# Optimization experiments

Measured on AMD Instinct MI355X. Metric: run time of the kernel, lower is better.

## Reference

```python
import jax, jax.numpy as jnp
import numpy as np

B, N, D = 64, 784, 768
H, HD, G = 32, 24, 2
HID = 3072
SCALE = HD ** -0.5
EPS = 1e-6


def _ln(x, g, b):
    m = jnp.mean(x, -1, keepdims=True)
    v = jnp.mean((x - m) ** 2, -1, keepdims=True)
    return (x - m) * jax.lax.rsqrt(v + EPS) * g + b


def setup_inputs() -> dict:
    key = jax.random.key(0)
    ks = jax.random.split(key, 12)
    def rn(k, shape, s=0.02):
        return (jax.random.normal(k, shape) * s).astype(jnp.float32)
    return {
        'x_cls': jax.random.normal(ks[0], (B, 1, D), jnp.float32),
        'x_img': jax.random.normal(ks[1], (B, N, D), jnp.float32),
        'ln1_g': jnp.ones((D,), jnp.float32), 'ln1_b': jnp.zeros((D,), jnp.float32),
        'Wq': rn(ks[2], (D, D)), 'bq': jnp.zeros((D,), jnp.float32),
        'Wk': rn(ks[3], (D, D)), 'bk': jnp.zeros((D,), jnp.float32),
        'Wv': rn(ks[4], (D, D)), 'bv': jnp.zeros((D,), jnp.float32),
        'w1_W': rn(ks[5], (H, H), 0.1), 'w1_b': jnp.zeros((H,), jnp.float32),
        'w2_W': rn(ks[6], (H, H), 0.1), 'w2_b': jnp.zeros((H,), jnp.float32),
        'proj_W': rn(ks[7], (D, D)), 'proj_b': jnp.zeros((D,), jnp.float32),
        'ln2_g': jnp.ones((D,), jnp.float32), 'ln2_b': jnp.zeros((D,), jnp.float32),
        'fc1_W': rn(ks[8], (G, HID // G, D // G)), 'fc1_b': jnp.zeros((G, HID // G), jnp.float32),
        'fc2_W': rn(ks[9], (G, D // G, HID // G)), 'fc2_b': jnp.zeros((G, D // G), jnp.float32),
    }


def reference(x_cls, x_img, ln1_g, ln1_b, Wq, bq, Wk, bk, Wv, bv,
              w1_W, w1_b, w2_W, w2_b, proj_W, proj_b, ln2_g, ln2_b,
              fc1_W, fc1_b, fc2_W, fc2_b):
    # --- ClassAttention (non-mismatch path), dropout = identity (eval) ---
    u = jnp.concatenate([x_cls, x_img], axis=1)  # [B, M, D], M = N+1
    M = u.shape[1]
    n = _ln(u, ln1_g, ln1_b)
    q = ((n[:, :1] @ Wq + bq).reshape(B, 1, H, HD).transpose(0, 2, 1, 3)) * SCALE  # [B,H,1,HD]
    k = (n @ Wk + bk).reshape(B, M, H, HD).transpose(0, 2, 1, 3)                   # [B,H,M,HD]
    v = (n @ Wv + bv).reshape(B, M, H, HD).transpose(0, 2, 1, 3)
    attn = jnp.einsum('bhqd,bhkd->bhqk', q, k)  # [B,H,1,M]
    # interactive score mixing across heads (w1 pre-softmax, w2 post-softmax)
    attn = attn + jnp.einsum('bhqk,hg->bgqk', attn, w1_W) + w1_b[None, :, None, None]
    attn = jax.nn.softmax(attn, axis=-1)
    attn = attn + jnp.einsum('bhqk,hg->bgqk', attn, w2_W) + w2_b[None, :, None, None]
    o = jnp.einsum('bhqk,bhkd->bhqd', attn, v).transpose(0, 2, 1, 3).reshape(B, 1, D)
    x_cls = x_cls + (o @ proj_W + proj_b)
    # --- GroupConvMlp on the cls token (grouped 1x1 convs + channel shuffle) ---
    y = _ln(x_cls, ln2_g, ln2_b)
    h = jnp.einsum('btgc,goc->btgo', y.reshape(B, 1, G, D // G), fc1_W) + fc1_b  # group-major out channels
    h = jax.nn.gelu(h.reshape(B, 1, HID), approximate=False)
    # channel_shuffle(group=G): out channel b*gc+a = in channel a*G+b
    h = h.reshape(B, 1, HID // G, G).transpose(0, 1, 3, 2).reshape(B, 1, HID)
    z = jnp.einsum('btgc,goc->btgo', h.reshape(B, 1, G, HID // G), fc2_W) + fc2_b
    x_cls = x_cls + z.reshape(B, 1, D)
    return (x_cls, x_img)
```

## Files before the change

### kernel.cpp

```cpp
#include <hip/hip_runtime.h>
#include <hip/hip_bf16.h>
#include <math.h>

#define BB   64
#define NN   784
#define DD   768
#define HH   32
#define HD24 24
#define MM   785
#define HIDN 3072
#define QSCALE 0.20412414523193154f
#define LNEPS 1e-6f

#define WS_Q     0
#define WS_RS    49152
#define WS_RM    100352
#define WS_S1P   151552
#define WS_BQP   163840
#define WS_LMX   176128
#define WS_LSM   184320
#define WS_A2P   192512
#define WS_WMP   200704
#define WS_PS    208896
#define WS_C1    210432
#define WS_H2    259584
#define WS_O     456192
#define WS_E     505344
#define WS_T     2143744
#define WS_T2    3751424
#define WS_SLQ   5359104
#define WS_KSEND 5563904
#define WS_ZP    0

typedef __attribute__((ext_vector_type(8))) short bf16x8;
typedef __attribute__((ext_vector_type(4))) float f32x4;

__device__ __forceinline__ unsigned packbf(float a, float b) {
  union { __hip_bfloat162 h2; unsigned u; } cv;
  cv.h2 = __float22bfloat162_rn(make_float2(a, b));
  return cv.u;
}

__global__ __launch_bounds__(256) void k_q(
    const float* __restrict__ x_cls,
    const float* __restrict__ g1, const float* __restrict__ b1,
    const float* __restrict__ Wq, const float* __restrict__ bq,
    float* __restrict__ ws)
{
  const int b = blockIdx.y;
  const int oc0 = blockIdx.x * 64;
  const int t = threadIdx.x;
  const int lane = t & 63, wid = t >> 6;

  __shared__ __align__(16) float nc_l[DD];
  __shared__ float red4[4][64];
  __shared__ float rS[4], rQ[4];
  __shared__ float musd[2];

  float xv[3];
  float s = 0.f, q2 = 0.f;
#pragma unroll
  for (int k = 0; k < 3; ++k) {
    float v = x_cls[(size_t)b * DD + t + 256 * k];
    xv[k] = v; s += v; q2 += v * v;
  }
#pragma unroll
  for (int off = 1; off < 64; off <<= 1) { s += __shfl_xor(s, off); q2 += __shfl_xor(q2, off); }
  if (lane == 0) { rS[wid] = s; rQ[wid] = q2; }
  __syncthreads();
  if (t == 0) {
    float ss = rS[0] + rS[1] + rS[2] + rS[3];
    float qq = rQ[0] + rQ[1] + rQ[2] + rQ[3];
    float mu = ss * (1.f / DD);
    musd[0] = mu; musd[1] = rsqrtf(qq * (1.f / DD) - mu * mu + LNEPS);
  }
  __syncthreads();
  {
    float mu = musd[0], rs = musd[1];
#pragma unroll
    for (int k = 0; k < 3; ++k) {
      int d = t + 256 * k;
      nc_l[d] = (xv[k] - mu) * rs * g1[d] + b1[d];
    }
  }
  __syncthreads();

  const int oc = t & 63, ks = t >> 6;
  const float* wp = Wq + (size_t)(ks * 192) * DD + oc0 + oc;
  const float* ncp = nc_l + ks * 192;
  float a0 = 0.f, a1 = 0.f, a2 = 0.f, a3 = 0.f;
#pragma unroll 4
  for (int d = 0; d < 192; d += 4) {
    a0 += ncp[d + 0] * wp[(size_t)(d + 0) * DD];
    a1 += ncp[d + 1] * wp[(size_t)(d + 1) * DD];
    a2 += ncp[d + 2] * wp[(size_t)(d + 2) * DD];
    a3 += ncp[d + 3] * wp[(size_t)(d + 3) * DD];
  }
  red4[ks][oc] = (a0 + a1) + (a2 + a3);
  __syncthreads();
  if (t < 64) {
    int ocg = oc0 + t;
    ws[WS_Q + (size_t)b * DD + ocg] =
        (red4[0][t] + red4[1][t] + red4[2][t] + red4[3][t] + bq[ocg]) * QSCALE;
  }
}

__global__ __launch_bounds__(256) void k_gqk(
    const float* __restrict__ g1, const float* __restrict__ b1,
    const float* __restrict__ Wk, const float* __restrict__ w1W,
    float* __restrict__ ws)
{
  const int b = blockIdx.y;
  const int d0 = blockIdx.x * 128;
  const int t = threadIdx.x;

  __shared__ __align__(16) float q_l[DD];
  __shared__ float T1[HH * HH];
  __shared__ float qk_l[128][33];
  __shared__ float pS[8][HH], pB[8][HH];

  for (int i = t; i < DD; i += 256) q_l[i] = ws[WS_Q + (size_t)b * DD + i];
  for (int i = t; i < HH * HH; i += 256) {
    int g = i >> 5, h = i & 31;
    T1[i] = w1W[i] + ((g == h) ? 1.f : 0.f);
  }
  __syncthreads();

  {
    const int dl = t >> 1, gh = t & 1;
    const float4* wr = (const float4*)(Wk + (size_t)(d0 + dl) * DD + gh * 384);
    const float4* qr = (const float4*)(q_l + gh * 384);
#pragma unroll 4
    for (int gg = 0; gg < 16; ++gg) {
      float a = 0.f;
#pragma unroll
      for (int c = 0; c < 6; ++c) {
        float4 w = wr[gg * 6 + c];
        float4 p = qr[gg * 6 + c];
        a += w.x * p.x + w.y * p.y + w.z * p.z + w.w * p.w;
      }
      qk_l[dl][gh * 16 + gg] = a;
    }
  }
  __syncthreads();
  {
    const int h = t & 31, dg = t >> 5;
    float fb[16];
    float s1a = 0.f, bqa = 0.f;
#pragma unroll 2
    for (int dd = 0; dd < 16; ++dd) {
      int dl = dg * 16 + dd;
      float f = 0.f;
#pragma unroll 8
      for (int g = 0; g < HH; ++g) f += qk_l[dl][g] * T1[g * HH + h];
      float gq = g1[d0 + dl] * f;
      fb[dd] = gq;
      s1a += gq;
      bqa += b1[d0 + dl] * qk_l[dl][h];
    }
    const int kstep = (d0 >> 5) + (dg >> 1);
    const int nt = h >> 4;
    const int lane0 = (h & 15) + 32 * (dg & 1);
    uint4* GQB = (uint4*)(ws + WS_E) + (size_t)b * (24 * 2 * 64);
    GQB[(kstep * 2 + nt) * 64 + lane0] =
        make_uint4(packbf(fb[0], fb[1]), packbf(fb[2], fb[3]),
                   packbf(fb[4], fb[5]), packbf(fb[6], fb[7]));
    GQB[(kstep * 2 + nt) * 64 + lane0 + 16] =
        make_uint4(packbf(fb[8], fb[9]), packbf(fb[10], fb[11]),
                   packbf(fb[12], fb[13]), packbf(fb[14], fb[15]));
    pS[dg][h] = s1a; pB[dg][h] = bqa;
  }
  __syncthreads();
  if (t < HH) {
    float s = 0.f, bq = 0.f;
#pragma unroll
    for (int k = 0; k < 8; ++k) { s += pS[k][t]; bq += pB[k][t]; }
    ws[WS_S1P + ((size_t)b * 6 + blockIdx.x) * HH + t] = s;
    ws[WS_BQP + ((size_t)b * 6 + blockIdx.x) * HH + t] = bq;
  }
}

__global__ __launch_bounds__(256) void k_main1(
    const float* __restrict__ x_cls, const float* __restrict__ x_img,
    float* __restrict__ ws)
{
  const int b = blockIdx.y;
  const int m0 = blockIdx.x * 64;
  const int nz = gridDim.z;
  const int kh = blockIdx.z;
  const int t = threadIdx.x;
  const int w = t >> 6;
  const int l = t & 63;
  const int lg = l >> 4;
  const int lm = l & 15;

  const uint4* GQ = (const uint4*)(ws + WS_E) + (size_t)b * (24 * 2 * 64);

  const int arow = m0 + w * 16 + lm;
  const bool av = (arow < MM);
  const int arc = av ? arow : 0;
  const float* asrc = (arc == 0) ? (x_cls + (size_t)b * DD)
                                 : (x_img + ((size_t)b * NN + (arc - 1)) * DD);
  const int nk = 24 / nz;
  const int k0 = kh * nk;

  f32x4 acc0 = {0.f, 0.f, 0.f, 0.f};
  f32x4 acc1 = {0.f, 0.f, 0.f, 0.f};
  float sl = 0.f, sq = 0.f;

#pragma unroll 4
  for (int kst = k0; kst < k0 + nk; ++kst) {
    float4 a0 = make_float4(0.f, 0.f, 0.f, 0.f);
    float4 a1 = make_float4(0.f, 0.f, 0.f, 0.f);
    if (av) {
      a0 = *(const float4*)(asrc + kst * 32 + 8 * lg);
      a1 = *(const float4*)(asrc + kst * 32 + 8 * lg + 4);
    }
    sl += (a0.x + a0.y) + (a0.z + a0.w) + (a1.x + a1.y) + (a1.z + a1.w);
    sq += a0.x*a0.x + a0.y*a0.y + a0.z*a0.z + a0.w*a0.w
        + a1.x*a1.x + a1.y*a1.y + a1.z*a1.z + a1.w*a1.w;
    union { uint4 u; bf16x8 h; } ua, ub0, ub1;
    ua.u = make_uint4(packbf(a0.x, a0.y), packbf(a0.z, a0.w),
                      packbf(a1.x, a1.y), packbf(a1.z, a1.w));
    ub0.u = GQ[(kst * 2 + 0) * 64 + l];
    ub1.u = GQ[(kst * 2 + 1) * 64 + l];
    acc0 = __builtin_amdgcn_mfma_f32_16x16x32_bf16(ua.h, ub0.h, acc0, 0, 0, 0);
    acc1 = __builtin_amdgcn_mfma_f32_16x16x32_bf16(ua.h, ub1.h, acc1, 0, 0, 0);
  }

  sl += __shfl_xor(sl, 16); sl += __shfl_xor(sl, 32);
  sq += __shfl_xor(sq, 16); sq += __shfl_xor(sq, 32);
  if (lg == 0 && av) {
    if (nz == 1) {
      float mu = sl * (1.f / DD);
      float rs = rsqrtf(sq * (1.f / DD) - mu * mu + LNEPS);
      ws[WS_RS + (size_t)b * 800 + arow] = rs;
      ws[WS_RM + (size_t)b * 800 + arow] = rs * mu;
    } else {
      float* slq = ws + WS_SLQ + (((size_t)b * 2 + kh) * 800 + arow) * 2;
      slq[0] = sl; slq[1] = sq;
    }
  }

  float* tb = ws + (kh ? WS_T2 : WS_T) + (size_t)b * MM * HH;
#pragma unroll
  for (int r = 0; r < 4; ++r) {
    int row = m0 + w * 16 + 4 * lg + r;
    if (row < MM) {
      tb[(size_t)row * HH + lm] = acc0[r];
      tb[(size_t)row * HH + 16 + lm] = acc1[r];
    }
  }
}

__global__ __launch_bounds__(256) void k_sm_a(
    const float* __restrict__ bk,
    const float* __restrict__ w1W, const float* __restrict__ w1b,
    float* __restrict__ ws, int ksplit)
{
  const int cx = blockIdx.x, b = blockIdx.y;
  const int t = threadIdx.x;
  const int lane = t & 63, wid = t >> 6;

  __shared__ float T1[HH * HH];
  __shared__ float s1_sh[HH], c0_sh[HH], bq_sh[HH];
  __shared__ float red[4][HH];
  __shared__ float lmax_sh[HH];

  for (int i = t; i < HH * HH; i += 256) {
    int g = i >> 5, h = i & 31;
    T1[i] = w1W[i] + ((g == h) ? 1.f : 0.f);
  }
  if (t < HH) {
    float s1v = 0.f, bqv = 0.f;
#pragma unroll
    for (int p = 0; p < 6; ++p) {
      s1v += ws[WS_S1P + ((size_t)b * 6 + p) * HH + t];
      bqv += ws[WS_BQP + ((size_t)b * 6 + p) * HH + t];
    }
    const float* qp = ws + WS_Q + (size_t)b * DD + t * HD24;
#pragma unroll
    for (int j = 0; j < HD24; ++j) bqv += bk[t * HD24 + j] * qp[j];
    s1_sh[t] = s1v; bq_sh[t] = bqv;
  }
  __syncthreads();
  if (t < HH) {
    float c0 = w1b[t];
#pragma unroll
    for (int g = 0; g < HH; ++g) c0 += T1[g * HH + t] * bq_sh[g];
    c0_sh[t] = c0;
  }
  __syncthreads();

  const int m = cx * 256 + t;
  const bool vm = (m < MM);
  float a1[HH];
  if (vm) {
    const float* tb = ws + WS_T + ((size_t)b * MM + m) * HH;
    const float* tb2 = ws + WS_T2 + ((size_t)b * MM + m) * HH;
    float rs, rm;
    if (ksplit) {
      const float* slq = ws + WS_SLQ + ((size_t)b * 2 * 800 + m) * 2;
      float sl = slq[0] + slq[(size_t)800 * 2];
      float sq = slq[1] + slq[(size_t)800 * 2 + 1];
      float mu = sl * (1.f / DD);
      rs = rsqrtf(sq * (1.f / DD) - mu * mu + LNEPS);
      rm = rs * mu;
      ws[WS_RS + (size_t)b * 800 + m] = rs;
      ws[WS_RM + (size_t)b * 800 + m] = rm;
    } else {
      rs = ws[WS_RS + (size_t)b * 800 + m];
      rm = ws[WS_RM + (size_t)b * 800 + m];
    }
#pragma unroll
    for (int q = 0; q < 8; ++q) {
      float4 tv = *(const float4*)(tb + q * 4);
      if (ksplit) {
        float4 t2 = *(const float4*)(tb2 + q * 4);
        tv.x += t2.x; tv.y += t2.y; tv.z += t2.z; tv.w += t2.w;
      }
      a1[4*q+0] = rs * tv.x - rm * s1_sh[4*q+0] + c0_sh[4*q+0];
      a1[4*q+1] = rs * tv.y - rm * s1_sh[4*q+1] + c0_sh[4*q+1];
      a1[4*q+2] = rs * tv.z - rm * s1_sh[4*q+2] + c0_sh[4*q+2];
      a1[4*q+3] = rs * tv.w - rm * s1_sh[4*q+3] + c0_sh[4*q+3];
    }
  } else {
#pragma unroll
    for (int h = 0; h < HH; ++h) a1[h] = -3.0e38f;
  }
#pragma unroll
  for (int h = 0; h < HH; ++h) {
    float v = a1[h];
#pragma unroll
    for (int off = 1; off < 64; off <<= 1) v = fmaxf(v, __shfl_xor(v, off));
    if (lane == 0) red[wid][h] = v;
  }
  __syncthreads();
  if (t < HH) {
    float v = fmaxf(fmaxf(red[0][t], red[1][t]), fmaxf(red[2][t], red[3][t]));
    lmax_sh[t] = v;
    ws[WS_LMX + ((size_t)b * 4 + cx) * HH + t] = v;
  }
  __syncthreads();
  float* E = ws + WS_E + (size_t)b * (HH * 800);
  if (vm) {
#pragma unroll
    for (int h = 0; h < HH; ++h) {
      float e = __expf(a1[h] - lmax_sh[h]);
      a1[h] = e;
      E[(size_t)h * 800 + m] = e;
    }
  } else {
#pragma unroll
    for (int h = 0; h < HH; ++h) a1[h] = 0.f;
  }
#pragma unroll
  for (int h = 0; h < HH; ++h) {
    float v = a1[h];
#pragma unroll
    for (int off = 1; off < 64; off <<= 1) v += __shfl_xor(v, off);
    if (lane == 0) red[wid][h] = v;
  }
  __syncthreads();
  if (t < HH)
    ws[WS_LSM + ((size_t)b * 4 + cx) * HH + t] = red[0][t] + red[1][t] + red[2][t] + red[3][t];
}

__global__ __launch_bounds__(256) void k_sm_b(
    const float* __restrict__ w2W, const float* __restrict__ w2b,
    float* __restrict__ ws)
{
  const int cx = blockIdx.x, b = blockIdx.y;
  const int t = threadIdx.x;
  const int lane = t & 63, wid = t >> 6;

  __shared__ __align__(16) float T2s[HH * HH];
  __shared__ float inv_sh[HH], w2b_sh[HH];
  __shared__ float red[4][HH];

  if (t < HH) {
    float l0 = ws[WS_LMX + ((size_t)b * 4 + 0) * HH + t];
    float l1 = ws[WS_LMX + ((size_t)b * 4 + 1) * HH + t];
    float l2 = ws[WS_LMX + ((size_t)b * 4 + 2) * HH + t];
    float l3 = ws[WS_LMX + ((size_t)b * 4 + 3) * HH + t];
    float gmax = fmaxf(fmaxf(l0, l1), fmaxf(l2, l3));
    float s = ws[WS_LSM + ((size_t)b * 4 + 0) * HH + t] * __expf(l0 - gmax)
            + ws[WS_LSM + ((size_t)b * 4 + 1) * HH + t] * __expf(l1 - gmax)
            + ws[WS_LSM + ((size_t)b * 4 + 2) * HH + t] * __expf(l2 - gmax)
            + ws[WS_LSM + ((size_t)b * 4 + 3) * HH + t] * __expf(l3 - gmax);
    float lcx = (cx == 0) ? l0 : (cx == 1) ? l1 : (cx == 2) ? l2 : l3;
    inv_sh[t] = __expf(lcx - gmax) / s;
    w2b_sh[t] = w2b[t];
  }
  __syncthreads();
  for (int i = t; i < HH * HH; i += 256) {
    int g = i >> 5, h = i & 31;
    T2s[i] = (w2W[i] + ((g == h) ? 1.f : 0.f)) * inv_sh[g];
  }
  __syncthreads();

  const int m = cx * 256 + t;
  float* E = ws + WS_E + (size_t)b * (HH * 800);
  float4 av[8];
#pragma unroll
  for (int q = 0; q < 8; ++q) av[q] = make_float4(0.f,0.f,0.f,0.f);
  float rm = 0.f;
  if (m < MM) {
    float rs = ws[WS_RS + (size_t)b * 800 + m];
    rm = ws[WS_RM + (size_t)b * 800 + m];
#pragma unroll 4
    for (int g = 0; g < HH; ++g) {
      float eg = E[(size_t)g * 800 + m];
#pragma unroll
      for (int q = 0; q < 8; ++q) {
        float4 t2 = *(const float4*)&T2s[g * HH + q * 4];
        av[q].x += eg * t2.x; av[q].y += eg * t2.y;
        av[q].z += eg * t2.z; av[q].w += eg * t2.w;
      }
    }
#pragma unroll
    for (int q = 0; q < 8; ++q) {
      av[q].x += w2b_sh[q*4+0]; av[q].y += w2b_sh[q*4+1];
      av[q].z += w2b_sh[q*4+2]; av[q].w += w2b_sh[q*4+3];
      E[(size_t)(q*4+0) * 800 + m] = av[q].x * rs;
      E[(size_t)(q*4+1) * 800 + m] = av[q].y * rs;
      E[(size_t)(q*4+2) * 800 + m] = av[q].z * rs;
      E[(size_t)(q*4+3) * 800 + m] = av[q].w * rs;
    }
  } else if (m < 800) {
#pragma unroll
    for (int h = 0; h < HH; ++h) E[(size_t)h * 800 + m] = 0.f;
  }
#pragma unroll
  for (int h = 0; h < HH; ++h) {
    float v = ((const float*)&av[h >> 2])[h & 3];
#pragma unroll
    for (int off = 1; off < 64; off <<= 1) v += __shfl_xor(v, off);
    if (lane == 0) red[wid][h] = v;
  }
  __syncthreads();
  if (t < HH)
    ws[WS_A2P + ((size_t)b * 4 + cx) * HH + t] = red[0][t] + red[1][t] + red[2][t] + red[3][t];
  __syncthreads();
#pragma unroll
  for (int h = 0; h < HH; ++h) {
    float v = ((const float*)&av[h >> 2])[h & 3] * rm;
#pragma unroll
    for (int off = 1; off < 64; off <<= 1) v += __shfl_xor(v, off);
    if (lane == 0) red[wid][h] = v;
  }
  __syncthreads();
  if (t < HH)
    ws[WS_WMP + ((size_t)b * 4 + cx) * HH + t] = red[0][t] + red[1][t] + red[2][t] + red[3][t];
}

__global__ __launch_bounds__(512) void k_wsum(
    const float* __restrict__ x_cls, const float* __restrict__ x_img,
    float* __restrict__ out, float* __restrict__ ws)
{
  const int b = blockIdx.y;
  const int d0 = blockIdx.x * 64;
  const int t = threadIdx.x;
  const int wv = t >> 6;
  const int mh = wv >> 2;
  const int hw = wv & 3;
  const int hb = hw * 8;
  const int dseg = t & 15;
  const int msub = (t >> 4) & 3;
  const int mcBeg = mh * 13;
  const int mcN = 13 - mh;

  __shared__ __align__(16) float w_l[HH][800];
  __shared__ __align__(16) float r_s[HH][68];

  const float* W = ws + WS_E + (size_t)b * (HH * 800);
  float* out_img = out + (size_t)BB * DD;

  {
    const float4* Wf = (const float4*)W;
    float4* wl4 = (float4*)&w_l[0][0];
    for (int i = t; i < (HH * 800) / 4; i += 512) wl4[i] = Wf[i];
  }
  __syncthreads();

  float acc[8][4];
#pragma unroll
  for (int j = 0; j < 8; ++j)
#pragma unroll
    for (int c = 0; c < 4; ++c) acc[j][c] = 0.f;

  float4 pu[8], pun[8];

  auto LOADU = [&](int j, float4* dst) {
#pragma unroll
    for (int i = 0; i < 8; ++i) {
      int m = (mcBeg + j) * 32 + msub * 8 + i;
      if (m < MM) {
        const float* src = (m == 0) ? (x_cls + (size_t)b * DD)
                                    : (x_img + ((size_t)b * NN + (m - 1)) * DD);
        dst[i] = *(const float4*)(src + d0 + dseg * 4);
      } else dst[i] = make_float4(0.f,0.f,0.f,0.f);
    }
  };

  LOADU(0, pu);
  for (int j = 0; j < mcN; ++j) {
    if (j + 1 < mcN) LOADU(j + 1, pun);
    const int mbase = (mcBeg + j) * 32 + msub * 8;
#pragma unroll
    for (int jj = 0; jj < 8; ++jj) {
      float4 wA = *(const float4*)&w_l[hb + jj][mbase];
      float4 wB = *(const float4*)&w_l[hb + jj][mbase + 4];
      float wv0 = wA.x, wv1 = wA.y, wv2 = wA.z, wv3 = wA.w;
      float wv4 = wB.x, wv5 = wB.y, wv6 = wB.z, wv7 = wB.w;
      acc[jj][0] += wv0*pu[0].x + wv1*pu[1].x + wv2*pu[2].x + wv3*pu[3].x
                  + wv4*pu[4].x + wv5*pu[5].x + wv6*pu[6].x + wv7*pu[7].x;
      acc[jj][1] += wv0*pu[0].y + wv1*pu[1].y + wv2*pu[2].y + wv3*pu[3].y
                  + wv4*pu[4].y + wv5*pu[5].y + wv6*pu[6].y + wv7*pu[7].y;
      acc[jj][2] += wv0*pu[0].z + wv1*pu[1].z + wv2*pu[2].z + wv3*pu[3].z
                  + wv4*pu[4].z + wv5*pu[5].z + wv6*pu[6].z + wv7*pu[7].z;
      acc[jj][3] += wv0*pu[0].w + wv1*pu[1].w + wv2*pu[2].w + wv3*pu[3].w
                  + wv4*pu[4].w + wv5*pu[5].w + wv6*pu[6].w + wv7*pu[7].w;
    }
#pragma unroll
    for (int i = 0; i < 8; ++i) {
      if ((i >> 1) == hw) {
        int m = (mcBeg + j) * 32 + msub * 8 + i;
        if (m >= 1 && m < MM)
          *(float4*)(out_img + ((size_t)b * NN + (m - 1)) * DD + d0 + dseg * 4) = pu[i];
      }
    }
    if (j + 1 < mcN) {
#pragma unroll
      for (int i = 0; i < 8; ++i) pu[i] = pun[i];
    }
  }

#pragma unroll
  for (int j = 0; j < 8; ++j)
#pragma unroll
    for (int c = 0; c < 4; ++c) {
      float v = acc[j][c];
      v += __shfl_xor(v, 16);
      v += __shfl_xor(v, 32);
      acc[j][c] = v;
    }
  __syncthreads();
  if (mh == 1 && msub == 0) {
#pragma unroll
    for (int j = 0; j < 8; ++j)
      *(float4*)&r_s[hb + j][dseg * 4] =
          make_float4(acc[j][0], acc[j][1], acc[j][2], acc[j][3]);
  }
  __syncthreads();
  if (mh == 0 && msub == 0) {
    float* R = ws + WS_T + (size_t)b * HH * DD;
#pragma unroll
    for (int j = 0; j < 8; ++j) {
      float4 rv = *(const float4*)&r_s[hb + j][dseg * 4];
      *(float4*)(R + (size_t)(hb + j) * DD + d0 + dseg * 4) =
          make_float4(acc[j][0] + rv.x, acc[j][1] + rv.y,
                      acc[j][2] + rv.z, acc[j][3] + rv.w);
    }
  }
}

__global__ __launch_bounds__(192) void k_att_o(
    const float* __restrict__ g1, const float* __restrict__ b1,
    const float* __restrict__ Wv, const float* __restrict__ bv,
    float* __restrict__ ws)
{
  const int h = blockIdx.x;
  const int b = blockIdx.y;
  const int t = threadIdx.x;

  __shared__ __align__(16) float agg_l[DD];
  __shared__ float red[8][25];
  __shared__ float a2wm[2];

  if (t == 0) {
    float a = 0.f;
#pragma unroll
    for (int c = 0; c < 4; ++c) a += ws[WS_A2P + ((size_t)b * 4 + c) * HH + h];
    a2wm[0] = a;
  }
  if (t == 1) {
    float w = 0.f;
#pragma unroll
    for (int c = 0; c < 4; ++c) w += ws[WS_WMP + ((size_t)b * 4 + c) * HH + h];
    a2wm[1] = w;
  }
  __syncthreads();
  const float A2 = a2wm[0], WM = a2wm[1];
  const float* R = ws + WS_T + ((size_t)b * HH + h) * DD;
  for (int i = t; i < DD; i += 192)
    agg_l[i] = g1[i] * (R[i] - WM) + b1[i] * A2;
  __syncthreads();

  const int oc = t % 24, ks = t / 24;
  const float* wv = Wv + (size_t)(ks * 96) * DD + h * HD24 + oc;
  const float* ag = agg_l + ks * 96;
  float a0 = 0.f, a1 = 0.f, a2 = 0.f, a3 = 0.f;
#pragma unroll 4
  for (int d = 0; d < 96; d += 4) {
    a0 += ag[d + 0] * wv[(size_t)(d + 0) * DD];
    a1 += ag[d + 1] * wv[(size_t)(d + 1) * DD];
    a2 += ag[d + 2] * wv[(size_t)(d + 2) * DD];
    a3 += ag[d + 3] * wv[(size_t)(d + 3) * DD];
  }
  red[ks][oc] = (a0 + a1) + (a2 + a3);
  __syncthreads();
  if (t < 24) {
    float o = A2 * bv[h * HD24 + t];
#pragma unroll
    for (int k = 0; k < 8; ++k) o += red[k][t];
    ws[WS_O + (size_t)b * DD + h * HD24 + t] = o;
  }
}

__global__ __launch_bounds__(256) void k_proj2(
    const float* __restrict__ x_cls,
    const float* __restrict__ projW, const float* __restrict__ projb,
    float* __restrict__ ws)
{
  const int b = blockIdx.y;
  const int oc0 = blockIdx.x * 64;
  const int t = threadIdx.x;

  __shared__ __align__(16) float o_l[DD];
  __shared__ float red4[4][64];

  for (int i = t; i < DD; i += 256) o_l[i] = ws[WS_O + (size_t)b * DD + i];
  __syncthreads();

  const int oc = t & 63, ks = t >> 6;
  const float* wp = projW + (size_t)(ks * 192) * DD + oc0 + oc;
  const float* op = o_l + ks * 192;
  float a0 = 0.f, a1 = 0.f, a2 = 0.f, a3 = 0.f;
#pragma unroll 4
  for (int d = 0; d < 192; d += 4) {
    a0 += op[d + 0] * wp[(size_t)(d + 0) * DD];
    a1 += op[d + 1] * wp[(size_t)(d + 1) * DD];
    a2 += op[d + 2] * wp[(size_t)(d + 2) * DD];
    a3 += op[d + 3] * wp[(size_t)(d + 3) * DD];
  }
  red4[ks][oc] = (a0 + a1) + (a2 + a3);
  __syncthreads();
  if (t < 64) {
    int ocg = oc0 + t;
    float c1 = red4[0][t] + red4[1][t] + red4[2][t] + red4[3][t]
             + projb[ocg] + x_cls[(size_t)b * DD + ocg];
    ws[WS_C1 + (size_t)b * DD + ocg] = c1;
    float cs = c1, cq = c1 * c1;
#pragma unroll
    for (int off = 1; off < 64; off <<= 1) { cs += __shfl_xor(cs, off); cq += __shfl_xor(cq, off); }
    if (t == 0) {
      ws[WS_PS + ((size_t)b * 12 + blockIdx.x) * 2 + 0] = cs;
      ws[WS_PS + ((size_t)b * 12 + blockIdx.x) * 2 + 1] = cq;
    }
  }
}

__global__ __launch_bounds__(256) void k_fc1(
    const float* __restrict__ fc1W, const float* __restrict__ fc1b,
    const float* __restrict__ g2, const float* __restrict__ b2,
    float* __restrict__ ws)
{
  const int g = blockIdx.x / 48;
  const int oc0 = (blockIdx.x % 48) * 32;
  const int t = threadIdx.x;
  const int txo = t & 7, tyb = t >> 3;

  __shared__ float y_s[64][65];
  __shared__ float w_s[32][65];
  __shared__ float mv[64][2];

  if (t < 64) {
    float s = 0.f, q = 0.f;
#pragma unroll
    for (int p = 0; p < 12; ++p) {
      s += ws[WS_PS + ((size_t)t * 12 + p) * 2 + 0];
      q += ws[WS_PS + ((size_t)t * 12 + p) * 2 + 1];
    }
    float mu = s * (1.f / DD);
    mv[t][0] = mu;
    mv[t][1] = rsqrtf(q * (1.f / DD) - mu * mu + LNEPS);
  }
  __syncthreads();

  float acc[2][4];
#pragma unroll
  for (int i = 0; i < 2; ++i)
#pragma unroll
    for (int j = 0; j < 4; ++j) acc[i][j] = 0.f;

#pragma unroll 1
  for (int kc = 0; kc < 6; ++kc) {
    {
      int r = t >> 2;
      float mu = mv[r][0], rs = mv[r][1];
#pragma unroll
      for (int p = 0; p < 4; ++p) {
        int c = (t & 3) * 4 + p * 16;
        int gc = g * 384 + kc * 64 + c;
        float4 v = *(const float4*)(ws + WS_C1 + (size_t)r * DD + gc);
        float4 gg = *(const float4*)(g2 + gc);
        float4 bb = *(const float4*)(b2 + gc);
        y_s[r][c+0] = (v.x - mu) * rs * gg.x + bb.x;
        y_s[r][c+1] = (v.y - mu) * rs * gg.y + bb.y;
        y_s[r][c+2] = (v.z - mu) * rs * gg.z + bb.z;
        y_s[r][c+3] = (v.w - mu) * rs * gg.w + bb.w;
      }
      int rw = t >> 3;
#pragma unroll
      for (int p = 0; p < 2; ++p) {
        int c = (t & 7) * 4 + p * 32;
        float4 w = *(const float4*)(fc1W + ((size_t)(g * 1536 + oc0 + rw)) * 384 + kc * 64 + c);
        w_s[rw][c+0] = w.x; w_s[rw][c+1] = w.y; w_s[rw][c+2] = w.z; w_s[rw][c+3] = w.w;
      }
    }
    __syncthreads();
#pragma unroll 4
    for (int kk = 0; kk < 64; ++kk) {
      float y0 = y_s[2*tyb+0][kk], y1 = y_s[2*tyb+1][kk];
      float w0 = w_s[4*txo+0][kk], w1 = w_s[4*txo+1][kk];
      float w2 = w_s[4*txo+2][kk], w3 = w_s[4*txo+3][kk];
      acc[0][0] += y0*w0; acc[0][1] += y0*w1; acc[0][2] += y0*w2; acc[0][3] += y0*w3;
      acc[1][0] += y1*w0; acc[1][1] += y1*w1; acc[1][2] += y1*w2; acc[1][3] += y1*w3;
    }
    __syncthreads();
  }

  float* H2 = ws + WS_H2;
#pragma unroll
  for (int i = 0; i < 2; ++i) {
    int bb = 2 * tyb + i;
#pragma unroll
    for (int j = 0; j < 4; ++j) {
      int oc = oc0 + 4 * txo + j;
      float v = acc[i][j] + fc1b[g * 1536 + oc];
      v = 0.5f * v * (1.f + erff(v * 0.70710678118654752f));
      H2[(size_t)bb * HIDN + (oc & 1) * 1536 + g * 768 + (oc >> 1)] = v;
    }
  }
}

__global__ __launch_bounds__(256) void k_fc2(
    const float* __restrict__ fc2W, float* __restrict__ ws)
{
  const int oc0 = blockIdx.x * 32;
  const int kq = blockIdx.y;
  const int g = blockIdx.z;
  const int t = threadIdx.x;
  const int txo = t & 7, tyb = t >> 3;

  __shared__ float h_s[64][65];
  __shared__ float w_s[32][65];

  float acc[2][4];
#pragma unroll
  for (int i = 0; i < 2; ++i)
#pragma unroll
    for (int j = 0; j < 4; ++j) acc[i][j] = 0.f;

  const float* H2 = ws + WS_H2;

#pragma unroll 1
  for (int kc = 0; kc < 6; ++kc) {
    {
      int r = t >> 2;
#pragma unroll
      for (int p = 0; p < 4; ++p) {
        int c = (t & 3) * 4 + p * 16;
        float4 v = *(const float4*)(H2 + (size_t)r * HIDN + g * 1536 + kq * 384 + kc * 64 + c);
        h_s[r][c+0] = v.x; h_s[r][c+1] = v.y; h_s[r][c+2] = v.z; h_s[r][c+3] = v.w;
      }
      int rw = t >> 3;
#pragma unroll
      for (int p = 0; p < 2; ++p) {
        int c = (t & 7) * 4 + p * 32;
        float4 w = *(const float4*)(fc2W + ((size_t)(g * 384 + oc0 + rw)) * 1536 + kq * 384 + kc * 64 + c);
        w_s[rw][c+0] = w.x; w_s[rw][c+1] = w.y; w_s[rw][c+2] = w.z; w_s[rw][c+3] = w.w;
      }
    }
    __syncthreads();
#pragma unroll 4
    for (int kk = 0; kk < 64; ++kk) {
      float y0 = h_s[2*tyb+0][kk], y1 = h_s[2*tyb+1][kk];
      float w0 = w_s[4*txo+0][kk], w1 = w_s[4*txo+1][kk];
      float w2 = w_s[4*txo+2][kk], w3 = w_s[4*txo+3][kk];
      acc[0][0] += y0*w0; acc[0][1] += y0*w1; acc[0][2] += y0*w2; acc[0][3] += y0*w3;
      acc[1][0] += y1*w0; acc[1][1] += y1*w1; acc[1][2] += y1*w2; acc[1][3] += y1*w3;
    }
    __syncthreads();
  }

  float* ZP = ws + WS_ZP + (size_t)kq * BB * DD;
#pragma unroll
  for (int i = 0; i < 2; ++i)
#pragma unroll
    for (int j = 0; j < 4; ++j)
      ZP[(size_t)(2 * tyb + i) * DD + g * 384 + oc0 + 4 * txo + j] = acc[i][j];
}

__global__ __launch_bounds__(256) void k_final(
    const float* __restrict__ fc2b, float* __restrict__ out, const float* __restrict__ ws)
{
  int idx = blockIdx.x * 256 + threadIdx.x;
  int d = idx % DD;
  float v = ws[WS_C1 + idx] + fc2b[d];
#pragma unroll
  for (int kq = 0; kq < 4; ++kq) v += ws[WS_ZP + (size_t)kq * BB * DD + idx];
  out[idx] = v;
}

extern "C" void kernel_launch(void* const* d_in, const int* in_sizes, int n_in,
                              void* d_out, int out_size, void* d_ws, size_t ws_size,
                              hipStream_t stream)
{
  (void)in_sizes; (void)n_in; (void)out_size;
  const float* x_cls = (const float*)d_in[0];
  const float* x_img = (const float*)d_in[1];
  const float* ln1_g = (const float*)d_in[2];
  const float* ln1_b = (const float*)d_in[3];
  const float* Wq    = (const float*)d_in[4];
  const float* bq    = (const float*)d_in[5];
  const float* Wk    = (const float*)d_in[6];
  const float* bk    = (const float*)d_in[7];
  const float* Wv    = (const float*)d_in[8];
  const float* bv    = (const float*)d_in[9];
  const float* w1W   = (const float*)d_in[10];
  const float* w1b   = (const float*)d_in[11];
  const float* w2W   = (const float*)d_in[12];
  const float* w2b   = (const float*)d_in[13];
  const float* projW = (const float*)d_in[14];
  const float* projb = (const float*)d_in[15];
  const float* ln2_g = (const float*)d_in[16];
  const float* ln2_b = (const float*)d_in[17];
  const float* fc1W  = (const float*)d_in[18];
  const float* fc1b  = (const float*)d_in[19];
  const float* fc2W  = (const float*)d_in[20];
  const float* fc2b  = (const float*)d_in[21];
  float* out = (float*)d_out;
  float* ws  = (float*)d_ws;

  const int ksplit = (ws_size >= (size_t)WS_KSEND * 4) ? 1 : 0;

  k_q    <<<dim3(12, 64), dim3(256), 0, stream>>>(x_cls, ln1_g, ln1_b, Wq, bq, ws);
  k_gqk  <<<dim3(6, 64),  dim3(256), 0, stream>>>(ln1_g, ln1_b, Wk, w1W, ws);
  k_main1<<<dim3(13, 64, ksplit ? 2 : 1), dim3(256), 0, stream>>>(x_cls, x_img, ws);
  k_sm_a <<<dim3(4, 64),  dim3(256), 0, stream>>>(bk, w1W, w1b, ws, ksplit);
  k_sm_b <<<dim3(4, 64),  dim3(256), 0, stream>>>(w2W, w2b, ws);
  k_wsum <<<dim3(12, 64), dim3(512), 0, stream>>>(x_cls, x_img, out, ws);
  k_att_o<<<dim3(32, 64), dim3(192), 0, stream>>>(ln1_g, ln1_b, Wv, bv, ws);
  k_proj2<<<dim3(12, 64), dim3(256), 0, stream>>>(x_cls, projW, projb, ws);
  k_fc1  <<<dim3(96),     dim3(256), 0, stream>>>(fc1W, fc1b, ln2_g, ln2_b, ws);
  k_fc2  <<<dim3(12, 4, 2), dim3(256), 0, stream>>>(fc2W, ws);
  k_final<<<dim3(192),    dim3(256), 0, stream>>>(fc2b, out, ws);
}
```

Measured before the change: 315.4 us.

## Stream attention weights through double-buffered LDS and split wsum across blocks

k_wsum no longer stages the full 32x800 weight matrix (about 100KB) in shared memory. It streams 32x32 weight chunks through a small double-buffered LDS tile, which should let more blocks share a CU. The two M-halves that were previously two wave groups of one 512-thread block now run as separate 256-thread blocks along grid z. Each half writes its partial sums to WS_T or WS_T2, and k_att_o adds the two. The costs are a barrier per chunk iteration and an extra workspace read in k_att_o.

After: 309.2 us. 2.0% less time.

```diff
diff --git a/kernel.cpp b/kernel.cpp
--- a/kernel.cpp
+++ b/kernel.cpp
@@ -454,35 +454,27 @@
     ws[WS_WMP + ((size_t)b * 4 + cx) * HH + t] = red[0][t] + red[1][t] + red[2][t] + red[3][t];
 }
 
-__global__ __launch_bounds__(512) void k_wsum(
+__global__ __launch_bounds__(256) void k_wsum(
     const float* __restrict__ x_cls, const float* __restrict__ x_img,
     float* __restrict__ out, float* __restrict__ ws)
 {
   const int b = blockIdx.y;
   const int d0 = blockIdx.x * 64;
-  const int t = threadIdx.x;
-  const int wv = t >> 6;
-  const int mh = wv >> 2;
-  const int hw = wv & 3;
-  const int hb = hw * 8;
+  const int nz = gridDim.z;
+  const int mh = blockIdx.z;
+  const int t = threadIdx.x;
   const int dseg = t & 15;
   const int msub = (t >> 4) & 3;
-  const int mcBeg = mh * 13;
-  const int mcN = 13 - mh;
-
-  __shared__ __align__(16) float w_l[HH][800];
-  __shared__ __align__(16) float r_s[HH][68];
+  const int hw = t >> 6;
+  const int hb = hw * 8;
+  const int mcBeg = (nz == 2) ? mh * 13 : 0;
+  const int mcN   = (nz == 2) ? (13 - mh) : 25;
+
+  __shared__ __align__(16) float w_s[2][HH][36];
 
   const float* W = ws + WS_E + (size_t)b * (HH * 800);
   float* out_img = out + (size_t)BB * DD;
 
-  {
-    const float4* Wf = (const float4*)W;
-    float4* wl4 = (float4*)&w_l[0][0];
-    for (int i = t; i < (HH * 800) / 4; i += 512) wl4[i] = Wf[i];
-  }
-  __syncthreads();
-
   float acc[8][4];
 #pragma unroll
   for (int j = 0; j < 8; ++j)
@@ -490,6 +482,7 @@
     for (int c = 0; c < 4; ++c) acc[j][c] = 0.f;
 
   float4 pu[8], pun[8];
+  float4 pwn;
 
   auto LOADU = [&](int j, float4* dst) {
 #pragma unroll
@@ -504,13 +497,22 @@
   };
 
   LOADU(0, pu);
+  {
+    float4 pw = *(const float4*)(W + (size_t)(t >> 3) * 800 + mcBeg * 32 + (t & 7) * 4);
+    *(float4*)&w_s[0][t >> 3][(t & 7) * 4] = pw;
+  }
+  __syncthreads();
+
   for (int j = 0; j < mcN; ++j) {
-    if (j + 1 < mcN) LOADU(j + 1, pun);
-    const int mbase = (mcBeg + j) * 32 + msub * 8;
+    if (j + 1 < mcN) {
+      pwn = *(const float4*)(W + (size_t)(t >> 3) * 800 + (mcBeg + j + 1) * 32 + (t & 7) * 4);
+      LOADU(j + 1, pun);
+    }
+    const float (*wc)[36] = w_s[j & 1];
 #pragma unroll
     for (int jj = 0; jj < 8; ++jj) {
-      float4 wA = *(const float4*)&w_l[hb + jj][mbase];
-      float4 wB = *(const float4*)&w_l[hb + jj][mbase + 4];
+      float4 wA = *(const float4*)&wc[hb + jj][msub * 8];
+      float4 wB = *(const float4*)&wc[hb + jj][msub * 8 + 4];
       float wv0 = wA.x, wv1 = wA.y, wv2 = wA.z, wv3 = wA.w;
       float wv4 = wB.x, wv5 = wB.y, wv6 = wB.z, wv7 = wB.w;
       acc[jj][0] += wv0*pu[0].x + wv1*pu[1].x + wv2*pu[2].x + wv3*pu[3].x
@@ -531,9 +533,11 @@
       }
     }
     if (j + 1 < mcN) {
+      *(float4*)&w_s[(j + 1) & 1][t >> 3][(t & 7) * 4] = pwn;
 #pragma unroll
       for (int i = 0; i < 8; ++i) pu[i] = pun[i];
     }
+    __syncthreads();
   }
 
 #pragma unroll
@@ -545,30 +549,19 @@
       v += __shfl_xor(v, 32);
       acc[j][c] = v;
     }
-  __syncthreads();
-  if (mh == 1 && msub == 0) {
+  if (msub == 0) {
+    float* R = ws + ((nz == 2 && mh == 1) ? WS_T2 : WS_T) + (size_t)b * HH * DD;
 #pragma unroll
     for (int j = 0; j < 8; ++j)
-      *(float4*)&r_s[hb + j][dseg * 4] =
+      *(float4*)(R + (size_t)(hb + j) * DD + d0 + dseg * 4) =
           make_float4(acc[j][0], acc[j][1], acc[j][2], acc[j][3]);
-  }
-  __syncthreads();
-  if (mh == 0 && msub == 0) {
-    float* R = ws + WS_T + (size_t)b * HH * DD;
-#pragma unroll
-    for (int j = 0; j < 8; ++j) {
-      float4 rv = *(const float4*)&r_s[hb + j][dseg * 4];
-      *(float4*)(R + (size_t)(hb + j) * DD + d0 + dseg * 4) =
-          make_float4(acc[j][0] + rv.x, acc[j][1] + rv.y,
-                      acc[j][2] + rv.z, acc[j][3] + rv.w);
-    }
   }
 }
 
 __global__ __launch_bounds__(192) void k_att_o(
     const float* __restrict__ g1, const float* __restrict__ b1,
     const float* __restrict__ Wv, const float* __restrict__ bv,
-    float* __restrict__ ws)
+    float* __restrict__ ws, int msplit)
 {
   const int h = blockIdx.x;
   const int b = blockIdx.y;
@@ -592,9 +585,12 @@
   }
   __syncthreads();
   const float A2 = a2wm[0], WM = a2wm[1];
-  const float* R = ws + WS_T + ((size_t)b * HH + h) * DD;
-  for (int i = t; i < DD; i += 192)
-    agg_l[i] = g1[i] * (R[i] - WM) + b1[i] * A2;
+  const float* R1 = ws + WS_T + ((size_t)b * HH + h) * DD;
+  const float* R2 = ws + WS_T2 + ((size_t)b * HH + h) * DD;
+  for (int i = t; i < DD; i += 192) {
+    float r = R1[i] + (msplit ? R2[i] : 0.f);
+    agg_l[i] = g1[i] * (r - WM) + b1[i] * A2;
+  }
   __syncthreads();
 
   const int oc = t % 24, ks = t / 24;
@@ -851,8 +847,8 @@
   k_main1<<<dim3(13, 64, ksplit ? 2 : 1), dim3(256), 0, stream>>>(x_cls, x_img, ws);
   k_sm_a <<<dim3(4, 64),  dim3(256), 0, stream>>>(bk, w1W, w1b, ws, ksplit);
   k_sm_b <<<dim3(4, 64),  dim3(256), 0, stream>>>(w2W, w2b, ws);
-  k_wsum <<<dim3(12, 64), dim3(512), 0, stream>>>(x_cls, x_img, out, ws);
-  k_att_o<<<dim3(32, 64), dim3(192), 0, stream>>>(ln1_g, ln1_b, Wv, bv, ws);
+  k_wsum <<<dim3(12, 64, ksplit ? 2 : 1), dim3(256), 0, stream>>>(x_cls, x_img, out, ws);
+  k_att_o<<<dim3(32, 64), dim3(192), 0, stream>>>(ln1_g, ln1_b, Wv, bv, ws, ksplit);
   k_proj2<<<dim3(12, 64), dim3(256), 0, stream>>>(x_cls, projW, projb, ws);
   k_fc1  <<<dim3(96),     dim3(256), 0, stream>>>(fc1W, fc1b, ln2_g, ln2_b, ws);
   k_fc2  <<<dim3(12, 4, 2), dim3(256), 0, stream>>>(fc2W, ws);
```
